# Performance work log

Measured on AMD Instinct MI355X. Metric: run time of the kernel, lower is better.

## Reference

```python
import jax, jax.numpy as jnp
import numpy as np

DIM = 256
HEADS = 4
HEAD_DIM = DIM // HEADS  # 64
SCALE = (DIM / HEADS) ** -0.5
EPS = 1e-5


def layer_norm(x, g, b):
    mu = jnp.mean(x, axis=-1, keepdims=True)
    var = jnp.mean(jnp.square(x - mu), axis=-1, keepdims=True)
    return (x - mu) * jax.lax.rsqrt(var + EPS) * g + b


def setup_inputs() -> dict:
    key = jax.random.key(0)
    ks = jax.random.split(key, 8)
    B, N, C = 2, 64 * 64, DIM
    H = 4 * DIM  # mlp hidden
    s = lambda fan: 1.0 / np.sqrt(fan)
    return {
        "x": jax.random.normal(ks[0], (B, N, C), jnp.float32),
        "w_qkv": jax.random.normal(ks[1], (C, 3 * C), jnp.float32) * s(C),
        "w_ao": jax.random.normal(ks[2], (C, C), jnp.float32) * s(C),
        "b_ao": jnp.zeros((C,), jnp.float32),
        "g_ao": jnp.ones((C,), jnp.float32),
        "be_ao": jnp.zeros((C,), jnp.float32),
        "g1": jnp.ones((C,), jnp.float32),
        "be1": jnp.zeros((C,), jnp.float32),
        "w_fc1": jax.random.normal(ks[3], (C, H), jnp.float32) * s(C),
        "b_fc1": jnp.zeros((H,), jnp.float32),
        "w_fc2": jax.random.normal(ks[4], (H, C), jnp.float32) * s(H),
        "b_fc2": jnp.zeros((C,), jnp.float32),
        "g2": jnp.ones((C,), jnp.float32),
        "be2": jnp.zeros((C,), jnp.float32),
    }


def reference(x, w_qkv, w_ao, b_ao, g_ao, be_ao, g1, be1,
              w_fc1, b_fc1, w_fc2, b_fc2, g2, be2):
    b, n, c = x.shape
    shortcut = x

    # --- LinearAttention ---
    qkv = x @ w_qkv  # [b, n, 3c]
    qkv = qkv.reshape(b, n, 3, HEADS, HEAD_DIM).transpose(2, 0, 3, 1, 4)  # [3,b,h,n,d]
    q, k, v = qkv[0], qkv[1], qkv[2]
    k = jax.nn.softmax(k, axis=-2)  # softmax over sequence dim
    q = q * SCALE
    context = jnp.einsum('bhid,bhjd->bhij', k, v)   # [b,h,n,n]
    out = jnp.einsum('bhij,bhid->bhjd', context, q)  # [b,h,n,d]
    out = out.reshape(b, n, c)  # faithful to torch reshape (no transpose)
    attn_out = layer_norm(out @ w_ao + b_ao, g_ao, be_ao)

    # --- block residuals ---
    h = shortcut + layer_norm(attn_out, g1, be1)
    mlp = jax.nn.gelu(h @ w_fc1 + b_fc1) @ w_fc2 + b_fc2
    h = h + layer_norm(mlp, g2, be2)
    return shortcut + h
```

## Files before the change

### kernel.cpp

```cpp
#include <hip/hip_runtime.h>

typedef __attribute__((ext_vector_type(8))) short short8;
typedef __attribute__((ext_vector_type(4))) float f32x4;

#define EPSF 1e-5f
#define NSEQ 4096
#define R_TOT 8192

__device__ __forceinline__ float bf2f(unsigned short u){
  union { unsigned int i; float f; } v; v.i = ((unsigned int)u) << 16; return v.f;
}
__device__ __forceinline__ unsigned short f2bf(float f){
  union { float f; unsigned int i; } v; v.f = f;
  unsigned int u = v.i;
  u += 0x7FFFu + ((u >> 16) & 1u);
  return (unsigned short)(u >> 16);
}
__device__ __forceinline__ float wsum(float v){
  #pragma unroll
  for (int o = 32; o > 0; o >>= 1) v += __shfl_xor(v, o, 64);
  return v;
}
__device__ __forceinline__ float gelu_tanh(float x){
  float y = 0.7978845608028654f * (x + 0.044715f * x * x * x);
  float e = __expf(2.0f * y);
  float th = 1.0f - 2.0f / (e + 1.0f);
  return 0.5f * x * (1.0f + th);
}
__device__ __forceinline__ void gload_lds16(const unsigned short* g, unsigned short* l){
  __builtin_amdgcn_global_load_lds(
      (const __attribute__((address_space(1))) unsigned int*)g,
      (__attribute__((address_space(3))) unsigned int*)l, 16, 0, 0);
}

__global__ void k_prep(const float* __restrict__ x, unsigned short* __restrict__ xbf,
                       const float* __restrict__ w_qkv, const float* __restrict__ w_ao,
                       const float* __restrict__ w_fc1, const float* __restrict__ w_fc2,
                       unsigned short* __restrict__ oq, unsigned short* __restrict__ oa,
                       unsigned short* __restrict__ o1, unsigned short* __restrict__ o2)
{
  int bid = blockIdx.x;
  const int t = threadIdx.x;
  if (bid < 2048){
    int i = (bid * 256 + t) * 4;
    float4 v = *(const float4*)(x + i);
    ushort4 o;
    o.x = f2bf(v.x); o.y = f2bf(v.y); o.z = f2bf(v.z); o.w = f2bf(v.w);
    *(ushort4*)(xbf + i) = o;
    return;
  }
  bid -= 2048;
  const float* in; unsigned short* out; int rows, cols, tid;
  if (bid < 48)      { in = w_qkv; out = oq; rows = 256;  cols = 768;  tid = bid; }
  else if (bid < 64) { in = w_ao;  out = oa; rows = 256;  cols = 256;  tid = bid - 48; }
  else if (bid < 128){ in = w_fc1; out = o1; rows = 256;  cols = 1024; tid = bid - 64; }
  else               { in = w_fc2; out = o2; rows = 1024; cols = 256;  tid = bid - 128; }
  const int tC = cols >> 6;
  const int r0 = (tid / tC) * 64, c0 = (tid % tC) * 64;
  __shared__ float tile[64][68];
  const int i = t >> 4, j4 = (t & 15) * 4;
  #pragma unroll
  for (int p = 0; p < 4; p++){
    float4 v = *(const float4*)(in + (size_t)(r0 + i + p * 16) * cols + c0 + j4);
    tile[i + p * 16][j4 + 0] = v.x; tile[i + p * 16][j4 + 1] = v.y;
    tile[i + p * 16][j4 + 2] = v.z; tile[i + p * 16][j4 + 3] = v.w;
  }
  __syncthreads();
  #pragma unroll
  for (int p = 0; p < 4; p++){
    int ci = i + p * 16;
    ushort4 o;
    o.x = f2bf(tile[j4 + 0][ci]); o.y = f2bf(tile[j4 + 1][ci]);
    o.z = f2bf(tile[j4 + 2][ci]); o.w = f2bf(tile[j4 + 3][ci]);
    *(ushort4*)(out + (size_t)(c0 + ci) * rows + r0 + j4) = o;
  }
}

template<int BM, int BN, bool HAS_BIAS, bool DO_GELU, bool OUT_BF16>
__global__ __launch_bounds__(256) void k_gemm(const unsigned short* __restrict__ A,
                       const unsigned short* __restrict__ BT,
                       const float* __restrict__ bias,
                       float* __restrict__ Cf,
                       unsigned short* __restrict__ Cb,
                       int M, int N, int K)
{
  constexpr int BK = 64;
  constexpr int FM = BM / 32, FN = BN / 32;
  __shared__ unsigned short As[BM * BK];
  __shared__ unsigned short Bs[BN * BK];
  const int t  = threadIdx.x;
  const int l  = t & 63;
  const int w  = t >> 6;
  const int wm = w >> 1, wn = w & 1;
  const int lr = l & 15, kq = l >> 4;
  const int m0 = blockIdx.y * BM, n0 = blockIdx.x * BN;

  f32x4 acc[FM][FN];
  #pragma unroll
  for (int i = 0; i < FM; i++)
    #pragma unroll
    for (int j = 0; j < FN; j++) acc[i][j] = (f32x4){0.f, 0.f, 0.f, 0.f};

  const int crow = l >> 3, ccolE = (l & 7) * 8;

  for (int k0 = 0; k0 < K; k0 += BK){
    #pragma unroll
    for (int c = w; c < BM / 8; c += 4)
      gload_lds16(A  + (size_t)(m0 + c * 8 + crow) * K + k0 + ccolE, As + c * 512);
    #pragma unroll
    for (int c = w; c < BN / 8; c += 4)
      gload_lds16(BT + (size_t)(n0 + c * 8 + crow) * K + k0 + ccolE, Bs + c * 512);
    __syncthreads();
    #pragma unroll
    for (int kk = 0; kk < BK; kk += 32){
      short8 af[FM], bfr[FN];
      #pragma unroll
      for (int i = 0; i < FM; i++)
        af[i]  = *(const short8*)&As[(wm * (BM / 2) + i * 16 + lr) * 64 + kk + kq * 8];
      #pragma unroll
      for (int j = 0; j < FN; j++)
        bfr[j] = *(const short8*)&Bs[(wn * (BN / 2) + j * 16 + lr) * 64 + kk + kq * 8];
      #pragma unroll
      for (int i = 0; i < FM; i++)
        #pragma unroll
        for (int j = 0; j < FN; j++)
          acc[i][j] = __builtin_amdgcn_mfma_f32_16x16x32_bf16(af[i], bfr[j], acc[i][j], 0, 0, 0);
    }
    __syncthreads();
  }

  const int row0 = m0 + wm * (BM / 2);
  const int col0 = n0 + wn * (BN / 2);
  #pragma unroll
  for (int i = 0; i < FM; i++){
    #pragma unroll
    for (int j = 0; j < FN; j++){
      #pragma unroll
      for (int r = 0; r < 4; r++){
        int row = row0 + i * 16 + kq * 4 + r;
        int col = col0 + j * 16 + lr;
        float v = acc[i][j][r];
        if (HAS_BIAS) v += bias[col];
        if (DO_GELU)  v = gelu_tanh(v);
        if (OUT_BF16) Cb[(size_t)row * N + col] = f2bf(v);
        else          Cf[(size_t)row * N + col] = v;
      }
    }
  }
}

#define NPAD 72
__global__ __launch_bounds__(64) void k_msum(const unsigned short* __restrict__ qkv,
                                             float* __restrict__ Spart,
                                             float* __restrict__ dsum_part)
{
  __shared__ unsigned short kT[64 * NPAD];
  __shared__ unsigned short qT[80 * NPAD];
  const int t = threadIdx.x;
  const int sl = blockIdx.x;
  const int bh = blockIdx.y;
  const int b = bh >> 2, h = bh & 3;
  const int e4 = (t & 15) * 4;
  const int nr = (t >> 4) * 4;
  #pragma unroll
  for (int it = 0; it < 4; ++it){
    int col = it * 16 + nr;
    int n = sl * 64 + col;
    const unsigned short* rp = qkv + (size_t)(b * NSEQ + n) * 768 + h * 64 + e4;
    ushort4 q0 = *(const ushort4*)(rp);
    ushort4 q1 = *(const ushort4*)(rp + 768);
    ushort4 q2 = *(const ushort4*)(rp + 1536);
    ushort4 q3 = *(const ushort4*)(rp + 2304);
    ushort4 k0 = *(const ushort4*)(rp + 256);
    ushort4 k1 = *(const ushort4*)(rp + 1024);
    ushort4 k2 = *(const ushort4*)(rp + 1792);
    ushort4 k3 = *(const ushort4*)(rp + 2560);
    ushort4 w;
    w.x = q0.x; w.y = q1.x; w.z = q2.x; w.w = q3.x; *(ushort4*)&qT[(e4+0)*NPAD + col] = w;
    w.x = q0.y; w.y = q1.y; w.z = q2.y; w.w = q3.y; *(ushort4*)&qT[(e4+1)*NPAD + col] = w;
    w.x = q0.z; w.y = q1.z; w.z = q2.z; w.w = q3.z; *(ushort4*)&qT[(e4+2)*NPAD + col] = w;
    w.x = q0.w; w.y = q1.w; w.z = q2.w; w.w = q3.w; *(ushort4*)&qT[(e4+3)*NPAD + col] = w;
    w.x = f2bf(__expf(bf2f(k0.x))); w.y = f2bf(__expf(bf2f(k1.x)));
    w.z = f2bf(__expf(bf2f(k2.x))); w.w = f2bf(__expf(bf2f(k3.x)));
    *(ushort4*)&kT[(e4+0)*NPAD + col] = w;
    w.x = f2bf(__expf(bf2f(k0.y))); w.y = f2bf(__expf(bf2f(k1.y)));
    w.z = f2bf(__expf(bf2f(k2.y))); w.w = f2bf(__expf(bf2f(k3.y)));
    *(ushort4*)&kT[(e4+1)*NPAD + col] = w;
    w.x = f2bf(__expf(bf2f(k0.z))); w.y = f2bf(__expf(bf2f(k1.z)));
    w.z = f2bf(__expf(bf2f(k2.z))); w.w = f2bf(__expf(bf2f(k3.z)));
    *(ushort4*)&kT[(e4+2)*NPAD + col] = w;
    w.x = f2bf(__expf(bf2f(k0.w))); w.y = f2bf(__expf(bf2f(k1.w)));
    w.z = f2bf(__expf(bf2f(k2.w))); w.w = f2bf(__expf(bf2f(k3.w)));
    *(ushort4*)&kT[(e4+3)*NPAD + col] = w;
  }
  if (t < 16){
    ushort4 ones; ones.x = 0x3F80; ones.y = 0x3F80; ones.z = 0x3F80; ones.w = 0x3F80;
    *(ushort4*)&qT[64 * NPAD + t * 4] = ones;
  }
  __syncthreads();
  const int lr = t & 15, kq = t >> 4;
  f32x4 acc[4][5];
  #pragma unroll
  for (int i = 0; i < 4; ++i)
    #pragma unroll
    for (int j = 0; j < 5; ++j) acc[i][j] = (f32x4){0.f, 0.f, 0.f, 0.f};
  #pragma unroll
  for (int ks = 0; ks < 2; ++ks){
    int nc = ks * 32 + kq * 8;
    short8 af[4], bf5[5];
    #pragma unroll
    for (int i = 0; i < 4; ++i) af[i] = *(const short8*)&kT[(i * 16 + lr) * NPAD + nc];
    #pragma unroll
    for (int j = 0; j < 5; ++j) bf5[j] = *(const short8*)&qT[(j * 16 + lr) * NPAD + nc];
    #pragma unroll
    for (int i = 0; i < 4; ++i)
      #pragma unroll
      for (int j = 0; j < 5; ++j)
        acc[i][j] = __builtin_amdgcn_mfma_f32_16x16x32_bf16(af[i], bf5[j], acc[i][j], 0, 0, 0);
  }
  float* sp = Spart + ((size_t)sl * 8 + bh) * 4096;
  #pragma unroll
  for (int i = 0; i < 4; ++i)
    #pragma unroll
    for (int j = 0; j < 4; ++j)
      #pragma unroll
      for (int r = 0; r < 4; ++r)
        sp[(i * 16 + kq * 4 + r) * 64 + j * 16 + lr] = acc[i][j][r];
  if (lr == 0){
    float* dp = dsum_part + (sl * 8 + bh) * 64;
    #pragma unroll
    for (int i = 0; i < 4; ++i)
      #pragma unroll
      for (int r = 0; r < 4; ++r)
        dp[i * 16 + kq * 4 + r] = acc[i][4][r];
  }
}

__global__ void k_mreduce(const float* __restrict__ Spart, const float* __restrict__ dsum_part,
                          float* __restrict__ Mm, float* __restrict__ dsumb){
  int bid = blockIdx.x, t = threadIdx.x;
  if (bid < 128){
    int idx = bid * 256 + t;
    float s = 0.f;
    #pragma unroll 8
    for (int sl = 0; sl < 64; ++sl) s += Spart[(size_t)sl * 32768 + idx];
    Mm[idx] = s;
  } else {
    int oi = (bid - 128) * 256 + t;
    float s = 0.f;
    #pragma unroll 8
    for (int sl = 0; sl < 64; ++sl) s += dsum_part[sl * 512 + oi];
    dsumb[oi] = s;
  }
}

__global__ __launch_bounds__(256) void k_projvm_dln(
    const unsigned short* __restrict__ qkv,
    const float* __restrict__ Mm, const float* __restrict__ dsumb,
    const unsigned short* __restrict__ waoT,
    const float* __restrict__ bias, const float* __restrict__ x,
    const float* __restrict__ g_ao, const float* __restrict__ be_ao,
    const float* __restrict__ g1, const float* __restrict__ be1,
    unsigned short* __restrict__ hbf, float* __restrict__ sxh)
{
  __shared__ __align__(16) char smem[16896 + 33280];
  unsigned short* As   = (unsigned short*)smem;
  unsigned short* vlds = (unsigned short*)(smem + 16896);
  unsigned short* mt   = (unsigned short*)(smem + 16896 + 16384);
  unsigned short* Bs   = (unsigned short*)(smem + 16896);
  float*          yt   = (float*)(smem + 16896);

  const int t = threadIdx.x, l = t & 63, w = t >> 6;
  const int lr = l & 15, kq = l >> 4;
  const int m0 = blockIdx.x * 32;
  const int b = m0 >> 12, h = (m0 >> 10) & 3;
  const int bh = b * 4 + h;
  const int n0 = (m0 & 1023) * 4;
  const int crow = l >> 3, ccolE = (l & 7) * 8;

  const unsigned short* vbase = qkv + (size_t)(b * NSEQ + n0) * 768 + 512 + h * 64;
  #pragma unroll
  for (int c = w; c < 16; c += 4)
    gload_lds16(vbase + (size_t)(c * 8 + crow) * 768 + ccolE, vlds + c * 512);
  {
    int e = t >> 2, d0 = (t & 3) * 16;
    float rdn = 0.125f / dsumb[bh * 64 + e];
    const float* mp = Mm + (size_t)bh * 4096 + e * 64 + d0;
    #pragma unroll
    for (int i = 0; i < 16; i += 4){
      float4 mv = *(const float4*)(mp + i);
      mt[(d0 + i + 0) * 64 + e] = f2bf(mv.x * rdn);
      mt[(d0 + i + 1) * 64 + e] = f2bf(mv.y * rdn);
      mt[(d0 + i + 2) * 64 + e] = f2bf(mv.z * rdn);
      mt[(d0 + i + 3) * 64 + e] = f2bf(mv.w * rdn);
    }
  }
  __syncthreads();
  {
    f32x4 vacc[2][4];
    #pragma unroll
    for (int i = 0; i < 2; i++)
      #pragma unroll
      for (int j = 0; j < 4; j++) vacc[i][j] = (f32x4){0.f, 0.f, 0.f, 0.f};
    #pragma unroll
    for (int kk = 0; kk < 64; kk += 32){
      short8 vf[2], mf[4];
      #pragma unroll
      for (int i = 0; i < 2; i++)
        vf[i] = *(const short8*)&vlds[((w * 2 + i) * 16 + lr) * 64 + kk + kq * 8];
      #pragma unroll
      for (int j = 0; j < 4; j++)
        mf[j] = *(const short8*)&mt[(j * 16 + lr) * 64 + kk + kq * 8];
      #pragma unroll
      for (int i = 0; i < 2; i++)
        #pragma unroll
        for (int j = 0; j < 4; j++)
          vacc[i][j] = __builtin_amdgcn_mfma_f32_16x16x32_bf16(vf[i], mf[j], vacc[i][j], 0, 0, 0);
    }
    #pragma unroll
    for (int i = 0; i < 2; i++)
      #pragma unroll
      for (int j = 0; j < 4; j++)
        #pragma unroll
        for (int r = 0; r < 4; r++)
          As[((w * 2 + i) * 4 + kq) * 264 + r * 64 + j * 16 + lr] = f2bf(vacc[i][j][r]);
  }
  __syncthreads();
  f32x4 acc[2][4];
  #pragma unroll
  for (int i = 0; i < 2; i++)
    #pragma unroll
    for (int j = 0; j < 4; j++) acc[i][j] = (f32x4){0.f, 0.f, 0.f, 0.f};
  for (int k0 = 0; k0 < 256; k0 += 64){
    #pragma unroll
    for (int c = w; c < 32; c += 4)
      gload_lds16(waoT + (size_t)(c * 8 + crow) * 256 + k0 + ccolE, Bs + c * 512);
    __syncthreads();
    #pragma unroll
    for (int kk = 0; kk < 64; kk += 32){
      short8 af[2], bfr[4];
      #pragma unroll
      for (int i = 0; i < 2; i++)
        af[i] = *(const short8*)&As[(i * 16 + lr) * 264 + k0 + kk + kq * 8];
      #pragma unroll
      for (int j = 0; j < 4; j++)
        bfr[j] = *(const short8*)&Bs[(w * 64 + j * 16 + lr) * 64 + kk + kq * 8];
      #pragma unroll
      for (int i = 0; i < 2; i++)
        #pragma unroll
        for (int j = 0; j < 4; j++)
          acc[i][j] = __builtin_amdgcn_mfma_f32_16x16x32_bf16(af[i], bfr[j], acc[i][j], 0, 0, 0);
    }
    __syncthreads();
  }
  #pragma unroll
  for (int i = 0; i < 2; i++)
    #pragma unroll
    for (int j = 0; j < 4; j++){
      float bv = bias[w * 64 + j * 16 + lr];
      #pragma unroll
      for (int r = 0; r < 4; r++)
        yt[(i * 16 + kq * 4 + r) * 260 + w * 64 + j * 16 + lr] = acc[i][j][r] + bv;
    }
  __syncthreads();
  const int gl = t & 63;
  #pragma unroll
  for (int rp = 0; rp < 8; rp++){
    int row = rp * 4 + (t >> 6);
    float4 v = *(const float4*)(yt + row * 260 + gl * 4);
    float mu = wsum(v.x + v.y + v.z + v.w) * 0.00390625f;
    float dx = v.x - mu, dy = v.y - mu, dz = v.z - mu, dw = v.w - mu;
    float rstd = rsqrtf(wsum(dx*dx + dy*dy + dz*dz + dw*dw) * 0.00390625f + EPSF);
    float4 ga = *(const float4*)(g_ao + gl * 4);
    float4 ba = *(const float4*)(be_ao + gl * 4);
    float zx = dx * rstd * ga.x + ba.x, zy = dy * rstd * ga.y + ba.y;
    float zz = dz * rstd * ga.z + ba.z, zw = dw * rstd * ga.w + ba.w;
    float mu2 = wsum(zx + zy + zz + zw) * 0.00390625f;
    float ex = zx - mu2, ey = zy - mu2, ez = zz - mu2, ew = zw - mu2;
    float rstd2 = rsqrtf(wsum(ex*ex + ey*ey + ez*ez + ew*ew) * 0.00390625f + EPSF);
    float4 gb = *(const float4*)(g1 + gl * 4);
    float4 bb = *(const float4*)(be1 + gl * 4);
    size_t off = (size_t)(m0 + row) * 256 + gl * 4;
    float4 xr = *(const float4*)(x + off);
    float hx = xr.x + ex * rstd2 * gb.x + bb.x;
    float hy = xr.y + ey * rstd2 * gb.y + bb.y;
    float hz = xr.z + ez * rstd2 * gb.z + bb.z;
    float hw = xr.w + ew * rstd2 * gb.w + bb.w;
    ushort4 hb; hb.x = f2bf(hx); hb.y = f2bf(hy); hb.z = f2bf(hz); hb.w = f2bf(hw);
    *(ushort4*)(hbf + off) = hb;
    float4 sv = {xr.x + hx, xr.y + hy, xr.z + hz, xr.w + hw};
    *(float4*)(sxh + off) = sv;
  }
}

__global__ __launch_bounds__(256) void k_fc2_ln(
    const unsigned short* __restrict__ A, const unsigned short* __restrict__ BT,
    const float* __restrict__ bias, const float* __restrict__ sxh,
    const float* __restrict__ g2, const float* __restrict__ be2,
    float* __restrict__ out)
{
  constexpr int K = 1024;
  __shared__ __align__(16) char smem[36864];
  unsigned short* As = (unsigned short*)smem;
  unsigned short* Bs = (unsigned short*)(smem + 4096);
  float* yt = (float*)smem;
  const int t = threadIdx.x, l = t & 63, w = t >> 6;
  const int lr = l & 15, kq = l >> 4;
  const int m0 = blockIdx.x * 32;
  const int crow = l >> 3, ccolE = (l & 7) * 8;
  f32x4 acc[2][4];
  #pragma unroll
  for (int i = 0; i < 2; i++)
    #pragma unroll
    for (int j = 0; j < 4; j++) acc[i][j] = (f32x4){0.f, 0.f, 0.f, 0.f};

  for (int k0 = 0; k0 < K; k0 += 64){
    gload_lds16(A + (size_t)(m0 + w * 8 + crow) * K + k0 + ccolE, As + w * 512);
    #pragma unroll
    for (int c = w; c < 32; c += 4)
      gload_lds16(BT + (size_t)(c * 8 + crow) * K + k0 + ccolE, Bs + c * 512);
    __syncthreads();
    #pragma unroll
    for (int kk = 0; kk < 64; kk += 32){
      short8 af[2], bfr[4];
      #pragma unroll
      for (int i = 0; i < 2; i++)
        af[i] = *(const short8*)&As[(i * 16 + lr) * 64 + kk + kq * 8];
      #pragma unroll
      for (int j = 0; j < 4; j++)
        bfr[j] = *(const short8*)&Bs[(w * 64 + j * 16 + lr) * 64 + kk + kq * 8];
      #pragma unroll
      for (int i = 0; i < 2; i++)
        #pragma unroll
        for (int j = 0; j < 4; j++)
          acc[i][j] = __builtin_amdgcn_mfma_f32_16x16x32_bf16(af[i], bfr[j], acc[i][j], 0, 0, 0);
    }
    __syncthreads();
  }
  #pragma unroll
  for (int i = 0; i < 2; i++)
    #pragma unroll
    for (int j = 0; j < 4; j++){
      float bv = bias[w * 64 + j * 16 + lr];
      #pragma unroll
      for (int r = 0; r < 4; r++)
        yt[(i * 16 + kq * 4 + r) * 260 + w * 64 + j * 16 + lr] = acc[i][j][r] + bv;
    }
  __syncthreads();
  const int gl = t & 63;
  #pragma unroll
  for (int rp = 0; rp < 8; rp++){
    int row = rp * 4 + (t >> 6);
    float4 v = *(const float4*)(yt + row * 260 + gl * 4);
    float mu = wsum(v.x + v.y + v.z + v.w) * 0.00390625f;
    float dx = v.x - mu, dy = v.y - mu, dz = v.z - mu, dw = v.w - mu;
    float rstd = rsqrtf(wsum(dx*dx + dy*dy + dz*dz + dw*dw) * 0.00390625f + EPSF);
    float4 g = *(const float4*)(g2 + gl * 4);
    float4 be = *(const float4*)(be2 + gl * 4);
    size_t off = (size_t)(m0 + row) * 256 + gl * 4;
    float4 sv = *(const float4*)(sxh + off);
    float4 o;
    o.x = sv.x + dx * rstd * g.x + be.x;
    o.y = sv.y + dy * rstd * g.y + be.y;
    o.z = sv.z + dz * rstd * g.z + be.z;
    o.w = sv.w + dw * rstd * g.w + be.w;
    *(float4*)(out + off) = o;
  }
}

extern "C" void kernel_launch(void* const* d_in, const int* in_sizes, int n_in,
                              void* d_out, int out_size, void* d_ws, size_t ws_size,
                              hipStream_t stream)
{
  const float* x     = (const float*)d_in[0];
  const float* w_qkv = (const float*)d_in[1];
  const float* w_ao  = (const float*)d_in[2];
  const float* b_ao  = (const float*)d_in[3];
  const float* g_ao  = (const float*)d_in[4];
  const float* be_ao = (const float*)d_in[5];
  const float* g1    = (const float*)d_in[6];
  const float* be1   = (const float*)d_in[7];
  const float* w_fc1 = (const float*)d_in[8];
  const float* b_fc1 = (const float*)d_in[9];
  const float* w_fc2 = (const float*)d_in[10];
  const float* b_fc2 = (const float*)d_in[11];
  const float* g2    = (const float*)d_in[12];
  const float* be2   = (const float*)d_in[13];
  float* out = (float*)d_out;
  char* ws = (char*)d_ws;

  unsigned short* qkv   = (unsigned short*)(ws + 0);
  unsigned short* xbf   = (unsigned short*)(ws + 12582912);
  unsigned short* wqkvT = (unsigned short*)(ws + 16777216);
  unsigned short* waoT  = (unsigned short*)(ws + 17170432);
  unsigned short* wfc1T = (unsigned short*)(ws + 17301504);
  unsigned short* wfc2T = (unsigned short*)(ws + 17825792);
  float* Spart = (float*)(ws + 18350080);
  float* dsum_part = (float*)(ws + 26738688);
  float* Mm    = (float*)(ws + 26869760);
  float* dsumb = (float*)(ws + 27000832);
  float* sxh   = (float*)(ws + 27004928);
  unsigned short* mlp1 = (unsigned short*)(ws + 35393536);

  k_prep<<<2240, 256, 0, stream>>>(x, xbf, w_qkv, w_ao, w_fc1, w_fc2,
                                   wqkvT, waoT, wfc1T, wfc2T);

  k_gemm<128, 128, false, false, true><<<dim3(6, 64), 256, 0, stream>>>(
      xbf, wqkvT, nullptr, nullptr, qkv, R_TOT, 768, 256);

  k_msum<<<dim3(64, 8), 64, 0, stream>>>(qkv, Spart, dsum_part);
  k_mreduce<<<130, 256, 0, stream>>>(Spart, dsum_part, Mm, dsumb);

  k_projvm_dln<<<256, 256, 0, stream>>>(qkv, Mm, dsumb, waoT, b_ao, x,
                                        g_ao, be_ao, g1, be1, xbf, sxh);

  k_gemm<128, 128, true, true, true><<<dim3(8, 64), 256, 0, stream>>>(
      xbf, wfc1T, b_fc1, nullptr, mlp1, R_TOT, 1024, 256);

  k_fc2_ln<<<256, 256, 0, stream>>>(mlp1, wfc2T, b_fc2, sxh, g2, be2, out);
}
```

Measured before the change: 83.10 us.

## Double-buffer LDS tiles in GEMM kernels and widen k_msum to four waves

Adds two-stage LDS double buffering to the generic GEMM, the output-projection GEMM in k_projvm_dln and the fc2+LayerNorm kernel, so the next K-slice's global-to-LDS loads are issued while the current slice is being multiplied. k_msum goes from one wave to four, with each wave computing a 16-row slice of the K^T·Q product to spread load and MFMA work. Shared memory per block grows substantially (for example about 106KB in k_projvm_dln), which can cut occupancy. The main loop's synchronization after prefetch is not fully visible, so buffer-reuse ordering carries some risk.

```diff
diff --git a/kernel.cpp b/kernel.cpp
--- a/kernel.cpp
+++ b/kernel.cpp
@@ -86,8 +86,8 @@
 {
   constexpr int BK = 64;
   constexpr int FM = BM / 32, FN = BN / 32;
-  __shared__ unsigned short As[BM * BK];
-  __shared__ unsigned short Bs[BN * BK];
+  __shared__ unsigned short As[2][BM * BK];
+  __shared__ unsigned short Bs[2][BN * BK];
   const int t  = threadIdx.x;
   const int l  = t & 63;
   const int w  = t >> 6;
@@ -102,24 +102,31 @@
     for (int j = 0; j < FN; j++) acc[i][j] = (f32x4){0.f, 0.f, 0.f, 0.f};
 
   const int crow = l >> 3, ccolE = (l & 7) * 8;
-
-  for (int k0 = 0; k0 < K; k0 += BK){
+  const int nk = K / BK;
+
+  auto stage = [&](int s, int bsel){
     #pragma unroll
     for (int c = w; c < BM / 8; c += 4)
-      gload_lds16(A  + (size_t)(m0 + c * 8 + crow) * K + k0 + ccolE, As + c * 512);
+      gload_lds16(A  + (size_t)(m0 + c * 8 + crow) * K + s * BK + ccolE, &As[bsel][c * 512]);
     #pragma unroll
     for (int c = w; c < BN / 8; c += 4)
-      gload_lds16(BT + (size_t)(n0 + c * 8 + crow) * K + k0 + ccolE, Bs + c * 512);
-    __syncthreads();
+      gload_lds16(BT + (size_t)(n0 + c * 8 + crow) * K + s * BK + ccolE, &Bs[bsel][c * 512]);
+  };
+
+  stage(0, 0);
+  __syncthreads();
+  for (int s = 0; s < nk; ++s){
+    const int cur = s & 1;
+    if (s + 1 < nk) stage(s + 1, cur ^ 1);
     #pragma unroll
     for (int kk = 0; kk < BK; kk += 32){
       short8 af[FM], bfr[FN];
       #pragma unroll
       for (int i = 0; i < FM; i++)
-        af[i]  = *(const short8*)&As[(wm * (BM / 2) + i * 16 + lr) * 64 + kk + kq * 8];
+        af[i]  = *(const short8*)&As[cur][(wm * (BM / 2) + i * 16 + lr) * 64 + kk + kq * 8];
       #pragma unroll
       for (int j = 0; j < FN; j++)
-        bfr[j] = *(const short8*)&Bs[(wn * (BN / 2) + j * 16 + lr) * 64 + kk + kq * 8];
+        bfr[j] = *(const short8*)&Bs[cur][(wn * (BN / 2) + j * 16 + lr) * 64 + kk + kq * 8];
       #pragma unroll
       for (int i = 0; i < FM; i++)
         #pragma unroll
@@ -150,9 +157,9 @@
 }
 
 #define NPAD 72
-__global__ __launch_bounds__(64) void k_msum(const unsigned short* __restrict__ qkv,
-                                             float* __restrict__ Spart,
-                                             float* __restrict__ dsum_part)
+__global__ __launch_bounds__(256) void k_msum(const unsigned short* __restrict__ qkv,
+                                              float* __restrict__ Spart,
+                                              float* __restrict__ dsum_part)
 {
   __shared__ unsigned short kT[64 * NPAD];
   __shared__ unsigned short qT[80 * NPAD];
@@ -161,10 +168,8 @@
   const int bh = blockIdx.y;
   const int b = bh >> 2, h = bh & 3;
   const int e4 = (t & 15) * 4;
-  const int nr = (t >> 4) * 4;
-  #pragma unroll
-  for (int it = 0; it < 4; ++it){
-    int col = it * 16 + nr;
+  const int col = (t >> 4) * 4;
+  {
     int n = sl * 64 + col;
     const unsigned short* rp = qkv + (size_t)(b * NSEQ + n) * 768 + h * 64 + e4;
     ushort4 q0 = *(const ushort4*)(rp);
@@ -198,41 +203,30 @@
     *(ushort4*)&qT[64 * NPAD + t * 4] = ones;
   }
   __syncthreads();
-  const int lr = t & 15, kq = t >> 4;
-  f32x4 acc[4][5];
-  #pragma unroll
-  for (int i = 0; i < 4; ++i)
-    #pragma unroll
-    for (int j = 0; j < 5; ++j) acc[i][j] = (f32x4){0.f, 0.f, 0.f, 0.f};
+  const int w4 = t >> 6, lr = t & 15, kq = (t >> 4) & 3;
+  f32x4 acc[5];
+  #pragma unroll
+  for (int j = 0; j < 5; ++j) acc[j] = (f32x4){0.f, 0.f, 0.f, 0.f};
   #pragma unroll
   for (int ks = 0; ks < 2; ++ks){
     int nc = ks * 32 + kq * 8;
-    short8 af[4], bf5[5];
-    #pragma unroll
-    for (int i = 0; i < 4; ++i) af[i] = *(const short8*)&kT[(i * 16 + lr) * NPAD + nc];
-    #pragma unroll
-    for (int j = 0; j < 5; ++j) bf5[j] = *(const short8*)&qT[(j * 16 + lr) * NPAD + nc];
-    #pragma unroll
-    for (int i = 0; i < 4; ++i)
-      #pragma unroll
-      for (int j = 0; j < 5; ++j)
-        acc[i][j] = __builtin_amdgcn_mfma_f32_16x16x32_bf16(af[i], bf5[j], acc[i][j], 0, 0, 0);
+    short8 af = *(const short8*)&kT[(w4 * 16 + lr) * NPAD + nc];
+    #pragma unroll
+    for (int j = 0; j < 5; ++j){
+      short8 bf = *(const short8*)&qT[(j * 16 + lr) * NPAD + nc];
+      acc[j] = __builtin_amdgcn_mfma_f32_16x16x32_bf16(af, bf, acc[j], 0, 0, 0);
+    }
   }
   float* sp = Spart + ((size_t)sl * 8 + bh) * 4096;
   #pragma unroll
-  for (int i = 0; i < 4; ++i)
-    #pragma unroll
-    for (int j = 0; j < 4; ++j)
-      #pragma unroll
-      for (int r = 0; r < 4; ++r)
-        sp[(i * 16 + kq * 4 + r) * 64 + j * 16 + lr] = acc[i][j][r];
+  for (int j = 0; j < 4; ++j)
+    #pragma unroll
+    for (int r = 0; r < 4; ++r)
+      sp[(w4 * 16 + kq * 4 + r) * 64 + j * 16 + lr] = acc[j][r];
   if (lr == 0){
     float* dp = dsum_part + (sl * 8 + bh) * 64;
     #pragma unroll
-    for (int i = 0; i < 4; ++i)
-      #pragma unroll
-      for (int r = 0; r < 4; ++r)
-        dp[i * 16 + kq * 4 + r] = acc[i][4][r];
+    for (int r = 0; r < 4; ++r) dp[w4 * 16 + kq * 4 + r] = acc[4][r];
   }
 }
 
@@ -263,12 +257,12 @@
     const float* __restrict__ g1, const float* __restrict__ be1,
     unsigned short* __restrict__ hbf, float* __restrict__ sxh)
 {
-  __shared__ __align__(16) char smem[16896 + 33280];
+  __shared__ __align__(16) char smem[16896 + 16384 + 8192 + 65536];
   unsigned short* As   = (unsigned short*)smem;
   unsigned short* vlds = (unsigned short*)(smem + 16896);
   unsigned short* mt   = (unsigned short*)(smem + 16896 + 16384);
-  unsigned short* Bs   = (unsigned short*)(smem + 16896);
-  float*          yt   = (float*)(smem + 16896);
+  unsigned short* Bs0  = (unsigned short*)(smem + 41472);
+  float*          yt   = (float*)(smem + 41472);
 
   const int t = threadIdx.x, l = t & 63, w = t >> 6;
   const int lr = l & 15, kq = l >> 4;
@@ -282,6 +276,9 @@
   #pragma unroll
   for (int c = w; c < 16; c += 4)
     gload_lds16(vbase + (size_t)(c * 8 + crow) * 768 + ccolE, vlds + c * 512);
+  #pragma unroll
+  for (int c = w; c < 32; c += 4)
+    gload_lds16(waoT + (size_t)(c * 8 + crow) * 256 + ccolE, Bs0 + c * 512);
   {
     int e = t >> 2, d0 = (t & 3) * 16;
     float rdn = 0.125f / dsumb[bh * 64 + e];
@@ -331,20 +328,25 @@
   for (int i = 0; i < 2; i++)
     #pragma unroll
     for (int j = 0; j < 4; j++) acc[i][j] = (f32x4){0.f, 0.f, 0.f, 0.f};
-  for (int k0 = 0; k0 < 256; k0 += 64){
-    #pragma unroll
-    for (int c = w; c < 32; c += 4)
-      gload_lds16(waoT + (size_t)(c * 8 + crow) * 256 + k0 + ccolE, Bs + c * 512);
-    __syncthreads();
+  for (int s = 0; s < 4; ++s){
+    const int cur = s & 1;
+    if (s + 1 < 4){
+      unsigned short* bnxt = Bs0 + (cur ^ 1) * 16384;
+      #pragma unroll
+      for (int c = w; c < 32; c += 4)
+        gload_lds16(waoT + (size_t)(c * 8 + crow) * 256 + (s + 1) * 64 + ccolE,
+                    bnxt + c * 512);
+    }
+    const unsigned short* bcur = Bs0 + cur * 16384;
     #pragma unroll
     for (int kk = 0; kk < 64; kk += 32){
       short8 af[2], bfr[4];
       #pragma unroll
       for (int i = 0; i < 2; i++)
-        af[i] = *(const short8*)&As[(i * 16 + lr) * 264 + k0 + kk + kq * 8];
+        af[i] = *(const short8*)&As[(i * 16 + lr) * 264 + s * 64 + kk + kq * 8];
       #pragma unroll
       for (int j = 0; j < 4; j++)
-        bfr[j] = *(const short8*)&Bs[(w * 64 + j * 16 + lr) * 64 + kk + kq * 8];
+        bfr[j] = *(const short8*)&bcur[(w * 64 + j * 16 + lr) * 64 + kk + kq * 8];
       #pragma unroll
       for (int i = 0; i < 2; i++)
         #pragma unroll
@@ -400,10 +402,10 @@
     float* __restrict__ out)
 {
   constexpr int K = 1024;
-  __shared__ __align__(16) char smem[36864];
-  unsigned short* As = (unsigned short*)smem;
-  unsigned short* Bs = (unsigned short*)(smem + 4096);
-  float* yt = (float*)smem;
+  __shared__ __align__(16) char smem[8192 + 65536];
+  unsigned short* As0 = (unsigned short*)smem;
+  unsigned short* Bs0 = (unsigned short*)(smem + 8192);
+  float* yt = (float*)(smem + 8192);
   const int t = threadIdx.x, l = t & 63, w = t >> 6;
   const int lr = l & 15, kq = l >> 4;
   const int m0 = blockIdx.x * 32;
@@ -414,21 +416,31 @@
     #pragma unroll
     for (int j = 0; j < 4; j++) acc[i][j] = (f32x4){0.f, 0.f, 0.f, 0.f};
 
-  for (int k0 = 0; k0 < K; k0 += 64){
-    gload_lds16(A + (size_t)(m0 + w * 8 + crow) * K + k0 + ccolE, As + w * 512);
+  auto stage = [&](int s, int bsel){
+    gload_lds16(A + (size_t)(m0 + w * 8 + crow) * K + s * 64 + ccolE,
+                As0 + bsel * 2048 + w * 512);
+    unsigned short* bdst = Bs0 + bsel * 16384;
     #pragma unroll
     for (int c = w; c < 32; c += 4)
-      gload_lds16(BT + (size_t)(c * 8 + crow) * K + k0 + ccolE, Bs + c * 512);
-    __syncthreads();
+      gload_lds16(BT + (size_t)(c * 8 + crow) * K + s * 64 + ccolE, bdst + c * 512);
+  };
+
+  stage(0, 0);
+  __syncthreads();
+  for (int s = 0; s < 16; ++s){
+    const int cur = s & 1;
+    if (s + 1 < 16) stage(s + 1, cur ^ 1);
+    const unsigned short* acur = As0 + cur * 2048;
+    const unsigned short* bcur = Bs0 + cur * 16384;
     #pragma unroll
     for (int kk = 0; kk < 64; kk += 32){
       short8 af[2], bfr[4];
       #pragma unroll
       for (int i = 0; i < 2; i++)
-        af[i] = *(const short8*)&As[(i * 16 + lr) * 64 + kk + kq * 8];
+        af[i] = *(const short8*)&acur[(i * 16 + lr) * 64 + kk + kq * 8];
       #pragma unroll
       for (int j = 0; j < 4; j++)
-        bfr[j] = *(const short8*)&Bs[(w * 64 + j * 16 + lr) * 64 + kk + kq * 8];
+        bfr[j] = *(const short8*)&bcur[(w * 64 + j * 16 + lr) * 64 + kk + kq * 8];
       #pragma unroll
       for (int i = 0; i < 2; i++)
         #pragma unroll
@@ -508,7 +520,7 @@
   k_gemm<128, 128, false, false, true><<<dim3(6, 64), 256, 0, stream>>>(
       xbf, wqkvT, nullptr, nullptr, qkv, R_TOT, 768, 256);
 
-  k_msum<<<dim3(64, 8), 64, 0, stream>>>(qkv, Spart, dsum_part);
+  k_msum<<<dim3(64, 8), 256, 0, stream>>>(qkv, Spart, dsum_part);
   k_mreduce<<<130, 256, 0, stream>>>(Spart, dsum_part, Mm, dsumb);
 
   k_projvm_dln<<<256, 256, 0, stream>>>(qkv, Mm, dsumb, waoT, b_ao, x,
```

Result: faster. 77.98 us (-6.2%).
